# Kernel tuning notes

Hardware: AMD Instinct MI355X
Metric: run time of the kernel (lower is better)

## Reference

```python
import math
import jax, jax.numpy as jnp
import numpy as np

BS, Q_LEN, DIM = 8, 16, 4096
MAX_SEQ = 4096
N_Q_HEADS, N_KV_HEADS, HEAD_DIM = 32, 8, 128
REP = N_Q_HEADS // N_KV_HEADS


def setup_inputs() -> dict:
    key = jax.random.key(0)
    ks = jax.random.split(key, 12)
    w = 0.02
    return {
        "x": jax.random.normal(ks[0], (BS, Q_LEN, DIM), jnp.float32),
        "k_cache": jax.random.normal(ks[1], (BS, MAX_SEQ, N_KV_HEADS, HEAD_DIM), jnp.float32),
        "v_cache": jax.random.normal(ks[2], (BS, MAX_SEQ, N_KV_HEADS, HEAD_DIM), jnp.float32),
        "Wq": jax.random.normal(ks[3], (DIM, N_Q_HEADS * HEAD_DIM), jnp.float32) * w,
        "bq": jax.random.normal(ks[4], (N_Q_HEADS * HEAD_DIM,), jnp.float32) * w,
        "Wk": jax.random.normal(ks[5], (DIM, N_KV_HEADS * HEAD_DIM), jnp.float32) * w,
        "bk": jax.random.normal(ks[6], (N_KV_HEADS * HEAD_DIM,), jnp.float32) * w,
        "Wv": jax.random.normal(ks[7], (DIM, N_KV_HEADS * HEAD_DIM), jnp.float32) * w,
        "bv": jax.random.normal(ks[8], (N_KV_HEADS * HEAD_DIM,), jnp.float32) * w,
        "Wo": jax.random.normal(ks[9], (N_Q_HEADS * HEAD_DIM, DIM), jnp.float32) * w,
        "bo": jax.random.normal(ks[10], (DIM,), jnp.float32) * w,
        "start_pos": MAX_SEQ - Q_LEN,
        "seq_len_for_kv": Q_LEN,
    }


def reference(x, k_cache, v_cache, Wq, bq, Wk, bk, Wv, bv, Wo, bo, start_pos, seq_len_for_kv):
    bs, sl, dim = x.shape
    # Projections (torch Linear: x @ W^T + b; here W stored as [in, out])
    q = (x @ Wq + bq).reshape(bs, sl, N_KV_HEADS, REP, HEAD_DIM)  # [b, q, g, r, d]
    k = (x @ Wk + bk).reshape(bs, sl, N_KV_HEADS, HEAD_DIM)
    v = (x @ Wv + bv).reshape(bs, sl, N_KV_HEADS, HEAD_DIM)
    # KV-cache append (start_pos / seq_len_for_kv are static Python ints)
    k_cache = k_cache.at[:, start_pos:start_pos + seq_len_for_kv].set(k)
    v_cache = v_cache.at[:, start_pos:start_pos + seq_len_for_kv].set(v)
    kv_len = start_pos + seq_len_for_kv
    keys = k_cache[:, :kv_len]    # [b, L, g, d]
    vals = v_cache[:, :kv_len]    # [b, L, g, d]
    # GQA: each kv head g serves REP query heads r (broadcast instead of repeat_kv)
    scale = 1.0 / math.sqrt(HEAD_DIM)
    scores = jnp.einsum('bqgrd,blgd->bgrql', q, keys) * scale  # [b, g, r, q, L]
    att = jax.nn.softmax(scores, axis=-1)
    out = jnp.einsum('bgrql,blgd->bqgrd', att, vals)           # [b, q, g, r, d]
    out = out.reshape(bs, sl, N_Q_HEADS * HEAD_DIM)
    return out @ Wo + bo
```

## Files before the change

### kernel.cpp

```cpp
#include <hip/hip_runtime.h>
#include <math.h>

#define DIM       4096
#define NKVH      8
#define HD        128
#define MAX_SEQ   4096
#define START_POS 4080
#define NQKV      6144
#define NCHUNK    8
#define CHUNK     512
#define KS        8
#define ATT_SCALE 0.08838834764831845f

#define WS_PART   0
#define WS_QH     6291456
#define WS_QL     6553600
#define WS_KNEW   6815744
#define WS_VNEW   6946816
#define WS_PM     7077888
#define WS_PL     7110656
#define WS_ATH    7143424
#define WS_ATL    7405568
#define WS_XH     7667712
#define WS_XL     7929856
#define WS_PARTO  WS_PART

typedef __bf16 bf16x8 __attribute__((ext_vector_type(8)));
typedef float  f32x4  __attribute__((ext_vector_type(4)));
typedef unsigned int uintx4 __attribute__((ext_vector_type(4)));

__device__ __forceinline__ unsigned short f2bf(float f) {
    return __builtin_bit_cast(unsigned short, (__bf16)f);
}
__device__ __forceinline__ float bf2f(unsigned short h) {
    union { unsigned int u; float f; } v; v.u = ((unsigned int)h) << 16;
    return v.f;
}
__device__ __forceinline__ void splitbf(float f, unsigned short &h, unsigned short &l) {
    h = f2bf(f);
    l = f2bf(f - bf2f(h));
}
__device__ __forceinline__ bf16x8 ldsfrag(const unsigned short* p) {
    uintx4 u = *(const uintx4*)p;
    return __builtin_bit_cast(bf16x8, u);
}
__device__ __forceinline__ bf16x8 ldsfrag2(const unsigned short* p) {
    union { uint2 u2[2]; bf16x8 v; } u;
    u.u2[0] = *(const uint2*)p;
    u.u2[1] = *(const uint2*)(p + 4);
    return u.v;
}
#define MFMA16(a,b,c) __builtin_amdgcn_mfma_f32_16x16x32_bf16(a, b, c, 0, 0, 0)
#define VCOMP(v,j) ((j)==0?(v).x:((j)==1?(v).y:((j)==2?(v).z:(v).w)))

__global__ __launch_bounds__(256) void split_x_kernel(
    const float* __restrict__ x, unsigned short* __restrict__ xh,
    unsigned short* __restrict__ xl, int n4)
{
    int i = blockIdx.x * 256 + threadIdx.x;
    if (i < n4) {
        float4 v = *(const float4*)(x + (size_t)i * 4);
        ushort4 h, l;
        splitbf(v.x, h.x, l.x);
        splitbf(v.y, h.y, l.y);
        splitbf(v.z, h.z, l.z);
        splitbf(v.w, h.w, l.w);
        *(ushort4*)(xh + (size_t)i * 4) = h;
        *(ushort4*)(xl + (size_t)i * 4) = l;
    }
}

template<int NT>
__device__ __forceinline__ void gemm_body(
    const unsigned short* __restrict__ Ah, const unsigned short* __restrict__ Al,
    const float* __restrict__ W, int ldW, int noff,
    float* __restrict__ part, int partStride, int ncol0, int ks,
    unsigned short* smem)
{
    unsigned short* Ahs = smem;
    unsigned short* Als = smem + 9216;
    unsigned short* Bs  = smem + 18432;
    constexpr int NC4   = NT * 4;
    constexpr int RSTEP = 256 / NC4;
    const int t = threadIdx.x;
    const int w = t >> 6, lane = t & 63, l15 = lane & 15, quad = lane >> 4;
    const int n4  = t & (NC4 - 1);
    const int kkw = t / NC4;

    f32x4 acc[2][NT];
    #pragma unroll
    for (int i = 0; i < 2; ++i)
        #pragma unroll
        for (int nt = 0; nt < NT; ++nt) acc[i][nt] = (f32x4){0.f, 0.f, 0.f, 0.f};

    const int k0base = ks * 512;
    uintx4 areg_h[4], areg_l[4];
    float4 wreg[NT];

    auto LOAD = [&](int it) {
        int k0 = k0base + it * 64;
        #pragma unroll
        for (int i = 0; i < 4; ++i) {
            int f = t + i * 256;
            int row = f >> 3, c0 = (f & 7) << 3;
            size_t off = (size_t)row * DIM + k0 + c0;
            areg_h[i] = *(const uintx4*)(Ah + off);
            areg_l[i] = *(const uintx4*)(Al + off);
        }
        #pragma unroll
        for (int i = 0; i < NT; ++i)
            wreg[i] = *(const float4*)(W + (size_t)(k0 + kkw + RSTEP * i) * ldW + noff + n4 * 4);
    };

    LOAD(0);
    for (int it = 0; it < 8; ++it) {
        __syncthreads();
        #pragma unroll
        for (int i = 0; i < 4; ++i) {
            int f = t + i * 256;
            int row = f >> 3, c0 = (f & 7) << 3;
            *(uintx4*)(Ahs + row * 72 + c0) = areg_h[i];
            *(uintx4*)(Als + row * 72 + c0) = areg_l[i];
        }
        #pragma unroll
        for (int i = 0; i < NT; ++i)
            #pragma unroll
            for (int j = 0; j < 4; ++j)
                Bs[(n4 * 4 + j) * 68 + kkw + RSTEP * i] = f2bf(VCOMP(wreg[i], j));
        __syncthreads();
        if (it < 7) LOAD(it + 1);
        #pragma unroll
        for (int kt = 0; kt < 2; ++kt) {
            int ko = kt * 32 + quad * 8;
            bf16x8 ah0 = ldsfrag(Ahs + ((2*w+0)*16 + l15) * 72 + ko);
            bf16x8 ah1 = ldsfrag(Ahs + ((2*w+1)*16 + l15) * 72 + ko);
            bf16x8 al0 = ldsfrag(Als + ((2*w+0)*16 + l15) * 72 + ko);
            bf16x8 al1 = ldsfrag(Als + ((2*w+1)*16 + l15) * 72 + ko);
            #pragma unroll
            for (int nt = 0; nt < NT; ++nt) {
                bf16x8 b = ldsfrag2(Bs + (nt*16 + l15) * 68 + ko);
                acc[0][nt] = MFMA16(ah0, b, acc[0][nt]);
                acc[0][nt] = MFMA16(al0, b, acc[0][nt]);
                acc[1][nt] = MFMA16(ah1, b, acc[1][nt]);
                acc[1][nt] = MFMA16(al1, b, acc[1][nt]);
            }
        }
    }

    constexpr int BN   = NT * 16;
    constexpr int EROW = BN + 4;
    float* eps = (float*)smem;
    #pragma unroll
    for (int i = 0; i < 2; ++i) {
        __syncthreads();
        #pragma unroll
        for (int nt = 0; nt < NT; ++nt)
            #pragma unroll
            for (int r = 0; r < 4; ++r)
                eps[(w*16 + quad*4 + r) * EROW + nt*16 + l15] = acc[i][nt][r];
        __syncthreads();
        #pragma unroll
        for (int s = 0; s < (64 * NC4) / 256; ++s) {
            int idx  = t + s * 256;
            int lrow = idx / NC4;
            int c4   = idx & (NC4 - 1);
            int grow = (2 * (lrow >> 4) + i) * 16 + (lrow & 15);
            f32x4 v = *(const f32x4*)&eps[lrow * EROW + c4 * 4];
            *(f32x4*)&part[(size_t)(ks * 128 + grow) * partStride + ncol0 + c4 * 4] = v;
        }
    }
}

__global__ __launch_bounds__(256, 2) void qkv_gemm_kernel(
    const unsigned short* __restrict__ xh, const unsigned short* __restrict__ xl,
    const float* __restrict__ Wq, const float* __restrict__ Wk,
    const float* __restrict__ Wv, float* __restrict__ part)
{
    __shared__ __align__(16) unsigned short smem[27136];
    int ncol0 = blockIdx.x * 128;
    int ks = blockIdx.y;
    const float* W; int ldW, noff;
    if (ncol0 < 4096)      { W = Wq; ldW = 4096; noff = ncol0; }
    else if (ncol0 < 5120) { W = Wk; ldW = 1024; noff = ncol0 - 4096; }
    else                   { W = Wv; ldW = 1024; noff = ncol0 - 5120; }
    gemm_body<8>(xh, xl, W, ldW, noff, part, NQKV, ncol0, ks, smem);
}

__global__ __launch_bounds__(256, 2) void oproj_gemm_kernel(
    const unsigned short* __restrict__ ah, const unsigned short* __restrict__ al,
    const float* __restrict__ Wo, float* __restrict__ part)
{
    __shared__ __align__(16) unsigned short smem[27136];
    int ncol0 = blockIdx.x * 128;
    int ks = blockIdx.y;
    gemm_body<8>(ah, al, Wo, 4096, ncol0, part, 4096, ncol0, ks, smem);
}

__global__ __launch_bounds__(256) void qkv_reduce_kernel(
    const float* __restrict__ part, const float* __restrict__ bq,
    const float* __restrict__ bk, const float* __restrict__ bv,
    unsigned short* __restrict__ qh, unsigned short* __restrict__ ql,
    float* __restrict__ k_new, float* __restrict__ v_new)
{
    int gid = blockIdx.x * 256 + threadIdx.x;
    int row = gid / 1536;
    int c4  = gid - row * 1536;
    int n = c4 * 4;
    float4 s = make_float4(0.f, 0.f, 0.f, 0.f);
    #pragma unroll
    for (int j = 0; j < KS; ++j) {
        float4 p = *(const float4*)&part[(size_t)(j * 128 + row) * NQKV + n];
        s.x += p.x; s.y += p.y; s.z += p.z; s.w += p.w;
    }
    if (n < 4096) {
        float4 b4 = *(const float4*)&bq[n];
        ushort4 h, l;
        splitbf(s.x + b4.x, h.x, l.x);
        splitbf(s.y + b4.y, h.y, l.y);
        splitbf(s.z + b4.z, h.z, l.z);
        splitbf(s.w + b4.w, h.w, l.w);
        *(ushort4*)&qh[row * 4096 + n] = h;
        *(ushort4*)&ql[row * 4096 + n] = l;
    } else if (n < 5120) {
        float4 b4 = *(const float4*)&bk[n - 4096];
        float4 o = make_float4(s.x + b4.x, s.y + b4.y, s.z + b4.z, s.w + b4.w);
        *(float4*)&k_new[row * 1024 + (n - 4096)] = o;
    } else {
        float4 b4 = *(const float4*)&bv[n - 5120];
        float4 o = make_float4(s.x + b4.x, s.y + b4.y, s.z + b4.z, s.w + b4.w);
        *(float4*)&v_new[row * 1024 + (n - 5120)] = o;
    }
}

__global__ __launch_bounds__(512, 2) void attn_partial5_kernel(
    const unsigned short* __restrict__ qhp, const unsigned short* __restrict__ qlp,
    const float* __restrict__ kc, const float* __restrict__ vc,
    const float* __restrict__ knew, const float* __restrict__ vnew,
    float* __restrict__ part_O, float* __restrict__ part_m, float* __restrict__ part_l)
{
    __shared__ unsigned short Kb[2][32][136];
    __shared__ unsigned short Vt[2][128][44];
    __shared__ unsigned short Pw[8][16 * 36];

    const int t = threadIdx.x;
    const int w = t >> 6, lane = t & 63, l15 = lane & 15, quad = lane >> 4;
    const int gsel = w >> 2;
    const int rep  = w & 3;
    const int blk = blockIdx.x;
    const int b = blk >> 5, gg = (blk >> 3) & 3, c = blk & 7;
    const int g = gg * 2 + gsel;

    const int p0 = t >> 6;
    const int q4 = t & 63;
    const int gl = q4 >> 5;
    const int d0 = (q4 & 31) << 2;

    bf16x8 qhf[4], qlf[4];
    {
        size_t base = (size_t)(b * 16 + l15) * DIM + (g * 4 + rep) * HD + quad * 8;
        #pragma unroll
        for (int kt = 0; kt < 4; ++kt) {
            qhf[kt] = ldsfrag(qhp + base + kt * 32);
            qlf[kt] = ldsfrag(qlp + base + kt * 32);
        }
    }

    float m_run[4], l_run[4];
    f32x4 oacc[8];
    #pragma unroll
    for (int r = 0; r < 4; ++r) { m_run[r] = -INFINITY; l_run[r] = 0.f; }
    #pragma unroll
    for (int d = 0; d < 8; ++d) oacc[d] = (f32x4){0.f, 0.f, 0.f, 0.f};

    float4 kreg[4], vreg[4];
    auto LOADKV = [&](int it) {
        #pragma unroll
        for (int i = 0; i < 4; ++i) {
            int pos = p0 + i * 8;
            int pg = c * CHUNK + it * 32 + pos;
            const float *ksrc, *vsrc;
            if (pg >= START_POS) {
                size_t off = (size_t)(b * 16 + pg - START_POS) * (NKVH * HD) + gg * 256 + q4 * 4;
                ksrc = knew + off; vsrc = vnew + off;
            } else {
                size_t off = ((size_t)(b * MAX_SEQ + pg) * NKVH) * HD + gg * 256 + q4 * 4;
                ksrc = kc + off; vsrc = vc + off;
            }
            kreg[i] = *(const float4*)ksrc;
            vreg[i] = *(const float4*)vsrc;
        }
    };

    unsigned short* phw = Pw[w];

    LOADKV(0);
    for (int it = 0; it < 16; ++it) {
        __syncthreads();
        #pragma unroll
        for (int i = 0; i < 4; ++i) {
            int pos = p0 + i * 8;
            ushort4 k4 = make_ushort4(f2bf(kreg[i].x), f2bf(kreg[i].y),
                                      f2bf(kreg[i].z), f2bf(kreg[i].w));
            *(ushort4*)&Kb[gl][pos][d0] = k4;
        }
        #pragma unroll
        for (int j = 0; j < 4; ++j) {
            ushort4 v4 = make_ushort4(f2bf(VCOMP(vreg[0], j)), f2bf(VCOMP(vreg[1], j)),
                                      f2bf(VCOMP(vreg[2], j)), f2bf(VCOMP(vreg[3], j)));
            *(ushort4*)&Vt[gl][d0 + j][p0 * 4] = v4;
        }
        __syncthreads();
        if (it + 1 < 16) LOADKV(it + 1);

        f32x4 sacc[2];
        sacc[0] = (f32x4){0.f,0.f,0.f,0.f};
        sacc[1] = (f32x4){0.f,0.f,0.f,0.f};
        #pragma unroll
        for (int nt = 0; nt < 2; ++nt)
            #pragma unroll
            for (int kt = 0; kt < 4; ++kt) {
                bf16x8 bh = ldsfrag(&Kb[gsel][nt*16 + l15][kt*32 + quad*8]);
                sacc[nt] = MFMA16(qhf[kt], bh, sacc[nt]);
                sacc[nt] = MFMA16(qlf[kt], bh, sacc[nt]);
            }

        float e0[4], e1[4], alpha[4];
        #pragma unroll
        for (int r = 0; r < 4; ++r) {
            float s0 = sacc[0][r] * ATT_SCALE;
            float s1 = sacc[1][r] * ATT_SCALE;
            float mx = fmaxf(s0, s1);
            mx = fmaxf(mx, __shfl_xor(mx, 1));
            mx = fmaxf(mx, __shfl_xor(mx, 2));
            mx = fmaxf(mx, __shfl_xor(mx, 4));
            mx = fmaxf(mx, __shfl_xor(mx, 8));
            float mnew = fmaxf(m_run[r], mx);
            alpha[r] = __expf(m_run[r] - mnew);
            e0[r] = __expf(s0 - mnew);
            e1[r] = __expf(s1 - mnew);
            float sum = e0[r] + e1[r];
            sum += __shfl_xor(sum, 1);
            sum += __shfl_xor(sum, 2);
            sum += __shfl_xor(sum, 4);
            sum += __shfl_xor(sum, 8);
            l_run[r] = l_run[r] * alpha[r] + sum;
            m_run[r] = mnew;
        }
        #pragma unroll
        for (int d = 0; d < 8; ++d)
            #pragma unroll
            for (int r = 0; r < 4; ++r) oacc[d][r] *= alpha[r];

        {
            int slot0 = 4 * (l15 & 7) + (l15 >> 3);
            #pragma unroll
            for (int r = 0; r < 4; ++r) {
                phw[(quad*4 + r) * 36 + slot0]     = f2bf(e0[r]);
                phw[(quad*4 + r) * 36 + slot0 + 2] = f2bf(e1[r]);
            }
        }
        bf16x8 pa = ldsfrag(phw + l15 * 36 + quad * 8);

        #pragma unroll
        for (int dt = 0; dt < 8; ++dt) {
            bf16x8 vb = ldsfrag(&Vt[gsel][dt*16 + l15][quad * 8]);
            oacc[dt] = MFMA16(pa, vb, oacc[dt]);
        }
    }

    const size_t obase = (size_t)((b * 8 + g) * 8 + c) * 64 + rep * 16 + quad * 4;
    #pragma unroll
    for (int dt = 0; dt < 8; ++dt)
        #pragma unroll
        for (int r = 0; r < 4; ++r)
            part_O[(obase + r) * HD + dt * 16 + l15] = oacc[dt][r];
    if (l15 == 0) {
        #pragma unroll
        for (int r = 0; r < 4; ++r) {
            part_m[obase + r] = m_run[r];
            part_l[obase + r] = l_run[r];
        }
    }
}

__global__ __launch_bounds__(128) void attn_combine_kernel(
    const float* __restrict__ part_O, const float* __restrict__ part_m,
    const float* __restrict__ part_l, unsigned short* __restrict__ ah,
    unsigned short* __restrict__ al)
{
    int bid = blockIdx.x;
    int d = threadIdx.x;
    int bg = bid >> 6;
    int row = bid & 63;
    float mc[NCHUNK], lc[NCHUNK];
    float M = -INFINITY;
    #pragma unroll
    for (int cc = 0; cc < NCHUNK; ++cc) {
        mc[cc] = part_m[(bg * NCHUNK + cc) * 64 + row];
        lc[cc] = part_l[(bg * NCHUNK + cc) * 64 + row];
        M = fmaxf(M, mc[cc]);
    }
    float L = 0.f, acc = 0.f;
    #pragma unroll
    for (int cc = 0; cc < NCHUNK; ++cc) {
        float wgt = __expf(mc[cc] - M);
        L += lc[cc] * wgt;
        acc += part_O[((size_t)(bg * NCHUNK + cc) * 64 + row) * HD + d] * wgt;
    }
    int b = bg >> 3, g = bg & 7;
    int r = row >> 4, qp = row & 15;
    float v = acc / L;
    unsigned short h, l; splitbf(v, h, l);
    size_t idx = (size_t)(b * 16 + qp) * DIM + (g * 4 + r) * HD + d;
    ah[idx] = h; al[idx] = l;
}

__global__ __launch_bounds__(256) void oproj_reduce_kernel(
    const float* __restrict__ part, const float* __restrict__ bo,
    float* __restrict__ out)
{
    int gid4 = blockIdx.x * 256 + threadIdx.x;
    int n = (gid4 & 1023) * 4;
    float4 s = make_float4(0.f, 0.f, 0.f, 0.f);
    #pragma unroll
    for (int j = 0; j < KS; ++j) {
        float4 p = *(const float4*)&part[(size_t)j * 524288 + (size_t)gid4 * 4];
        s.x += p.x; s.y += p.y; s.z += p.z; s.w += p.w;
    }
    float4 b4 = *(const float4*)&bo[n];
    float4 o = make_float4(s.x + b4.x, s.y + b4.y, s.z + b4.z, s.w + b4.w);
    *(float4*)&out[(size_t)gid4 * 4] = o;
}

extern "C" void kernel_launch(void* const* d_in, const int* in_sizes, int n_in,
                              void* d_out, int out_size, void* d_ws, size_t ws_size,
                              hipStream_t stream)
{
    const float* x  = (const float*)d_in[0];
    const float* kc = (const float*)d_in[1];
    const float* vc = (const float*)d_in[2];
    const float* Wq = (const float*)d_in[3];
    const float* bq = (const float*)d_in[4];
    const float* Wk = (const float*)d_in[5];
    const float* bk = (const float*)d_in[6];
    const float* Wv = (const float*)d_in[7];
    const float* bv = (const float*)d_in[8];
    const float* Wo = (const float*)d_in[9];
    const float* bo = (const float*)d_in[10];
    float* out = (float*)d_out;
    float* ws  = (float*)d_ws;

    unsigned short* xh = (unsigned short*)(ws + WS_XH);
    unsigned short* xl = (unsigned short*)(ws + WS_XL);
    unsigned short* qh = (unsigned short*)(ws + WS_QH);
    unsigned short* ql = (unsigned short*)(ws + WS_QL);
    unsigned short* ath = (unsigned short*)(ws + WS_ATH);
    unsigned short* atl = (unsigned short*)(ws + WS_ATL);

    split_x_kernel<<<512, 256, 0, stream>>>(x, xh, xl, 131072);
    qkv_gemm_kernel<<<dim3(48, KS), 256, 0, stream>>>(xh, xl, Wq, Wk, Wv, ws + WS_PART);
    qkv_reduce_kernel<<<768, 256, 0, stream>>>(ws + WS_PART, bq, bk, bv,
                                               qh, ql, ws + WS_KNEW, ws + WS_VNEW);
    attn_partial5_kernel<<<256, 512, 0, stream>>>(qh, ql, kc, vc,
                                                  ws + WS_KNEW, ws + WS_VNEW,
                                                  ws + WS_PARTO, ws + WS_PM, ws + WS_PL);
    attn_combine_kernel<<<4096, 128, 0, stream>>>(ws + WS_PARTO, ws + WS_PM,
                                                  ws + WS_PL, ath, atl);
    oproj_gemm_kernel<<<dim3(32, KS), 256, 0, stream>>>(ath, atl, Wo, ws + WS_PART);
    oproj_reduce_kernel<<<512, 256, 0, stream>>>(ws + WS_PART, bo, out);
}
```

Before: 440.0 us.

## Fuse activation bf16 split into GEMMs and double-buffer weight tile in LDS

Removes the separate split_x kernel and the hi/lo bf16 outputs of the attention combine. The GEMMs now read fp32 activations straight from global memory into registers and split them into hi/lo bf16 on the fly, with no LDS staging for A. The weight tile is double-buffered in LDS so only one barrier per k-step is needed, and the next tile is prefetched two steps ahead. The aim is to save a kernel launch, the activation round trips, and barrier stalls. The cost is repeated global reads and split arithmetic for A across column blocks, plus uncoalesced-style per-lane fragment loads.

Result: slower. 452.1 us (+2.7%).

```diff
diff --git a/kernel.cpp b/kernel.cpp
--- a/kernel.cpp
+++ b/kernel.cpp
@@ -19,15 +19,13 @@
 #define WS_VNEW   6946816
 #define WS_PM     7077888
 #define WS_PL     7110656
-#define WS_ATH    7143424
-#define WS_ATL    7405568
-#define WS_XH     7667712
-#define WS_XL     7929856
+#define WS_O      7143424
 #define WS_PARTO  WS_PART
 
 typedef __bf16 bf16x8 __attribute__((ext_vector_type(8)));
 typedef float  f32x4  __attribute__((ext_vector_type(4)));
 typedef unsigned int uintx4 __attribute__((ext_vector_type(4)));
+typedef unsigned short ushort8v __attribute__((ext_vector_type(8)));
 
 __device__ __forceinline__ unsigned short f2bf(float f) {
     return __builtin_bit_cast(unsigned short, (__bf16)f);
@@ -53,35 +51,16 @@
 #define MFMA16(a,b,c) __builtin_amdgcn_mfma_f32_16x16x32_bf16(a, b, c, 0, 0, 0)
 #define VCOMP(v,j) ((j)==0?(v).x:((j)==1?(v).y:((j)==2?(v).z:(v).w)))
 
-__global__ __launch_bounds__(256) void split_x_kernel(
-    const float* __restrict__ x, unsigned short* __restrict__ xh,
-    unsigned short* __restrict__ xl, int n4)
-{
-    int i = blockIdx.x * 256 + threadIdx.x;
-    if (i < n4) {
-        float4 v = *(const float4*)(x + (size_t)i * 4);
-        ushort4 h, l;
-        splitbf(v.x, h.x, l.x);
-        splitbf(v.y, h.y, l.y);
-        splitbf(v.z, h.z, l.z);
-        splitbf(v.w, h.w, l.w);
-        *(ushort4*)(xh + (size_t)i * 4) = h;
-        *(ushort4*)(xl + (size_t)i * 4) = l;
-    }
-}
-
 template<int NT>
 __device__ __forceinline__ void gemm_body(
-    const unsigned short* __restrict__ Ah, const unsigned short* __restrict__ Al,
+    const float* __restrict__ A,
     const float* __restrict__ W, int ldW, int noff,
     float* __restrict__ part, int partStride, int ncol0, int ks,
-    unsigned short* smem)
-{
-    unsigned short* Ahs = smem;
-    unsigned short* Als = smem + 9216;
-    unsigned short* Bs  = smem + 18432;
+    unsigned short* Bs)
+{
     constexpr int NC4   = NT * 4;
     constexpr int RSTEP = 256 / NC4;
+    constexpr int BUF   = NT * 16 * 68;
     const int t = threadIdx.x;
     const int w = t >> 6, lane = t & 63, l15 = lane & 15, quad = lane >> 4;
     const int n4  = t & (NC4 - 1);
@@ -94,62 +73,71 @@
         for (int nt = 0; nt < NT; ++nt) acc[i][nt] = (f32x4){0.f, 0.f, 0.f, 0.f};
 
     const int k0base = ks * 512;
-    uintx4 areg_h[4], areg_l[4];
     float4 wreg[NT];
 
-    auto LOAD = [&](int it) {
+    auto LOADW = [&](int it) {
         int k0 = k0base + it * 64;
-        #pragma unroll
-        for (int i = 0; i < 4; ++i) {
-            int f = t + i * 256;
-            int row = f >> 3, c0 = (f & 7) << 3;
-            size_t off = (size_t)row * DIM + k0 + c0;
-            areg_h[i] = *(const uintx4*)(Ah + off);
-            areg_l[i] = *(const uintx4*)(Al + off);
-        }
         #pragma unroll
         for (int i = 0; i < NT; ++i)
             wreg[i] = *(const float4*)(W + (size_t)(k0 + kkw + RSTEP * i) * ldW + noff + n4 * 4);
     };
-
-    LOAD(0);
+    auto STAGE = [&](int buf) {
+        #pragma unroll
+        for (int i = 0; i < NT; ++i)
+            #pragma unroll
+            for (int j = 0; j < 4; ++j)
+                Bs[buf * BUF + (n4 * 4 + j) * 68 + kkw + RSTEP * i] = f2bf(VCOMP(wreg[i], j));
+    };
+
+    LOADW(0);
+    STAGE(0);
+    LOADW(1);
+    __syncthreads();
+
     for (int it = 0; it < 8; ++it) {
+        if (it < 7) {
+            STAGE((it + 1) & 1);
+            if (it < 6) LOADW(it + 2);
+        }
+        const unsigned short* Bc = Bs + (it & 1) * BUF;
+        const int k0 = k0base + it * 64;
+        #pragma unroll
+        for (int kt = 0; kt < 2; ++kt) {
+            const int kc0 = k0 + kt * 32 + quad * 8;
+            bf16x8 ah[2], al[2];
+            #pragma unroll
+            for (int i = 0; i < 2; ++i) {
+                const float* ap = A + (size_t)((2 * w + i) * 16 + l15) * 4096 + kc0;
+                float4 x0 = *(const float4*)ap;
+                float4 x1 = *(const float4*)(ap + 4);
+                ushort8v h, l;
+                unsigned short hh, ll;
+                splitbf(x0.x, hh, ll); h[0] = hh; l[0] = ll;
+                splitbf(x0.y, hh, ll); h[1] = hh; l[1] = ll;
+                splitbf(x0.z, hh, ll); h[2] = hh; l[2] = ll;
+                splitbf(x0.w, hh, ll); h[3] = hh; l[3] = ll;
+                splitbf(x1.x, hh, ll); h[4] = hh; l[4] = ll;
+                splitbf(x1.y, hh, ll); h[5] = hh; l[5] = ll;
+                splitbf(x1.z, hh, ll); h[6] = hh; l[6] = ll;
+                splitbf(x1.w, hh, ll); h[7] = hh; l[7] = ll;
+                ah[i] = __builtin_bit_cast(bf16x8, h);
+                al[i] = __builtin_bit_cast(bf16x8, l);
+            }
+            #pragma unroll
+            for (int nt = 0; nt < NT; ++nt) {
+                bf16x8 b = ldsfrag2(Bc + (nt * 16 + l15) * 68 + kt * 32 + quad * 8);
+                acc[0][nt] = MFMA16(ah[0], b, acc[0][nt]);
+                acc[0][nt] = MFMA16(al[0], b, acc[0][nt]);
+                acc[1][nt] = MFMA16(ah[1], b, acc[1][nt]);
+                acc[1][nt] = MFMA16(al[1], b, acc[1][nt]);
+            }
+        }
         __syncthreads();
-        #pragma unroll
-        for (int i = 0; i < 4; ++i) {
-            int f = t + i * 256;
-            int row = f >> 3, c0 = (f & 7) << 3;
-            *(uintx4*)(Ahs + row * 72 + c0) = areg_h[i];
-            *(uintx4*)(Als + row * 72 + c0) = areg_l[i];
-        }
-        #pragma unroll
-        for (int i = 0; i < NT; ++i)
-            #pragma unroll
-            for (int j = 0; j < 4; ++j)
-                Bs[(n4 * 4 + j) * 68 + kkw + RSTEP * i] = f2bf(VCOMP(wreg[i], j));
-        __syncthreads();
-        if (it < 7) LOAD(it + 1);
-        #pragma unroll
-        for (int kt = 0; kt < 2; ++kt) {
-            int ko = kt * 32 + quad * 8;
-            bf16x8 ah0 = ldsfrag(Ahs + ((2*w+0)*16 + l15) * 72 + ko);
-            bf16x8 ah1 = ldsfrag(Ahs + ((2*w+1)*16 + l15) * 72 + ko);
-            bf16x8 al0 = ldsfrag(Als + ((2*w+0)*16 + l15) * 72 + ko);
-            bf16x8 al1 = ldsfrag(Als + ((2*w+1)*16 + l15) * 72 + ko);
-            #pragma unroll
-            for (int nt = 0; nt < NT; ++nt) {
-                bf16x8 b = ldsfrag2(Bs + (nt*16 + l15) * 68 + ko);
-                acc[0][nt] = MFMA16(ah0, b, acc[0][nt]);
-                acc[0][nt] = MFMA16(al0, b, acc[0][nt]);
-                acc[1][nt] = MFMA16(ah1, b, acc[1][nt]);
-                acc[1][nt] = MFMA16(al1, b, acc[1][nt]);
-            }
-        }
     }
 
     constexpr int BN   = NT * 16;
     constexpr int EROW = BN + 4;
-    float* eps = (float*)smem;
+    float* eps = (float*)Bs;
     #pragma unroll
     for (int i = 0; i < 2; ++i) {
         __syncthreads();
@@ -172,28 +160,28 @@
 }
 
 __global__ __launch_bounds__(256, 2) void qkv_gemm_kernel(
-    const unsigned short* __restrict__ xh, const unsigned short* __restrict__ xl,
+    const float* __restrict__ x,
     const float* __restrict__ Wq, const float* __restrict__ Wk,
     const float* __restrict__ Wv, float* __restrict__ part)
 {
-    __shared__ __align__(16) unsigned short smem[27136];
+    __shared__ __align__(16) unsigned short Bs[2 * 128 * 68];
     int ncol0 = blockIdx.x * 128;
     int ks = blockIdx.y;
     const float* W; int ldW, noff;
     if (ncol0 < 4096)      { W = Wq; ldW = 4096; noff = ncol0; }
     else if (ncol0 < 5120) { W = Wk; ldW = 1024; noff = ncol0 - 4096; }
     else                   { W = Wv; ldW = 1024; noff = ncol0 - 5120; }
-    gemm_body<8>(xh, xl, W, ldW, noff, part, NQKV, ncol0, ks, smem);
+    gemm_body<8>(x, W, ldW, noff, part, NQKV, ncol0, ks, Bs);
 }
 
 __global__ __launch_bounds__(256, 2) void oproj_gemm_kernel(
-    const unsigned short* __restrict__ ah, const unsigned short* __restrict__ al,
-    const float* __restrict__ Wo, float* __restrict__ part)
-{
-    __shared__ __align__(16) unsigned short smem[27136];
+    const float* __restrict__ O, const float* __restrict__ Wo,
+    float* __restrict__ part)
+{
+    __shared__ __align__(16) unsigned short Bs[2 * 128 * 68];
     int ncol0 = blockIdx.x * 128;
     int ks = blockIdx.y;
-    gemm_body<8>(ah, al, Wo, 4096, ncol0, part, 4096, ncol0, ks, smem);
+    gemm_body<8>(O, Wo, 4096, ncol0, part, 4096, ncol0, ks, Bs);
 }
 
 __global__ __launch_bounds__(256) void qkv_reduce_kernel(
@@ -385,8 +373,7 @@
 
 __global__ __launch_bounds__(128) void attn_combine_kernel(
     const float* __restrict__ part_O, const float* __restrict__ part_m,
-    const float* __restrict__ part_l, unsigned short* __restrict__ ah,
-    unsigned short* __restrict__ al)
+    const float* __restrict__ part_l, float* __restrict__ O)
 {
     int bid = blockIdx.x;
     int d = threadIdx.x;
@@ -409,10 +396,7 @@
     }
     int b = bg >> 3, g = bg & 7;
     int r = row >> 4, qp = row & 15;
-    float v = acc / L;
-    unsigned short h, l; splitbf(v, h, l);
-    size_t idx = (size_t)(b * 16 + qp) * DIM + (g * 4 + r) * HD + d;
-    ah[idx] = h; al[idx] = l;
+    O[(size_t)(b * 16 + qp) * DIM + (g * 4 + r) * HD + d] = acc / L;
 }
 
 __global__ __launch_bounds__(256) void oproj_reduce_kernel(
@@ -450,22 +434,18 @@
     float* out = (float*)d_out;
     float* ws  = (float*)d_ws;
 
-    unsigned short* xh = (unsigned short*)(ws + WS_XH);
-    unsigned short* xl = (unsigned short*)(ws + WS_XL);
     unsigned short* qh = (unsigned short*)(ws + WS_QH);
     unsigned short* ql = (unsigned short*)(ws + WS_QL);
-    unsigned short* ath = (unsigned short*)(ws + WS_ATH);
-    unsigned short* atl = (unsigned short*)(ws + WS_ATL);
-
-    split_x_kernel<<<512, 256, 0, stream>>>(x, xh, xl, 131072);
-    qkv_gemm_kernel<<<dim3(48, KS), 256, 0, stream>>>(xh, xl, Wq, Wk, Wv, ws + WS_PART);
+    float* O = ws + WS_O;
+
+    qkv_gemm_kernel<<<dim3(48, KS), 256, 0, stream>>>(x, Wq, Wk, Wv, ws + WS_PART);
     qkv_reduce_kernel<<<768, 256, 0, stream>>>(ws + WS_PART, bq, bk, bv,
                                                qh, ql, ws + WS_KNEW, ws + WS_VNEW);
     attn_partial5_kernel<<<256, 512, 0, stream>>>(qh, ql, kc, vc,
                                                   ws + WS_KNEW, ws + WS_VNEW,
                                                   ws + WS_PARTO, ws + WS_PM, ws + WS_PL);
     attn_combine_kernel<<<4096, 128, 0, stream>>>(ws + WS_PARTO, ws + WS_PM,
-                                                  ws + WS_PL, ath, atl);
-    oproj_gemm_kernel<<<dim3(32, KS), 256, 0, stream>>>(ath, atl, Wo, ws + WS_PART);
+                                                  ws + WS_PL, O);
+    oproj_gemm_kernel<<<dim3(32, KS), 256, 0, stream>>>(O, Wo, ws + WS_PART);
     oproj_reduce_kernel<<<512, 256, 0, stream>>>(ws + WS_PART, bo, out);
 }
```
